# Kernel optimization log

Hardware: AMD Instinct MI355X
Metric: run time of the kernel (lower is better)

The kernel has to match this reference:

```python
import jax, jax.numpy as jnp
import numpy as np

C_IN = 512
OUT_CH = 256  # query/key gate channels
DIM = 64      # squeeze/extraction rank


def setup_inputs() -> dict:
    key = jax.random.key(0)
    ks = jax.random.split(key, 11)
    b, c, h, w = 16, C_IN, 64, 64

    def winit(k, o, i):
        # torch Conv2d default init: U(-s, s), s = 1/sqrt(fan_in)
        s = 1.0 / np.sqrt(i)
        return jax.random.uniform(k, (o, i), jnp.float32, -s, s)

    return {
        "x": jax.random.normal(ks[0], (b, c, h, w), jnp.float32),
        "Wq": winit(ks[1], OUT_CH, C_IN), "bq": winit(ks[2], OUT_CH, C_IN)[:, 0],
        "Wk": winit(ks[3], OUT_CH, C_IN), "bk": winit(ks[4], OUT_CH, C_IN)[:, 0],
        "Wv": winit(ks[5], C_IN, C_IN),   "bv": winit(ks[6], C_IN, C_IN)[:, 0],
        "Ws": winit(ks[7], DIM, C_IN),    "bs": winit(ks[8], DIM, C_IN)[:, 0],
        "We": winit(ks[9], DIM, C_IN),    "be": winit(ks[10], DIM, C_IN)[:, 0],
    }


def reference(x, Wq, bq, Wk, bk, Wv, bv, Ws, bs, We, be):
    b, c, h, w = x.shape
    n = h * w
    xf = x.reshape(b, c, n)  # [b, 512, n] (1x1 conv == matmul over channels)

    Q = jnp.einsum('oc,bcn->bon', Wq, xf) + bq[:, None]   # [b, 256, n]
    K = jnp.einsum('oc,bcn->bon', Wk, xf) + bk[:, None]   # [b, 256, n]
    gate = jax.nn.sigmoid(jnp.mean(Q * K, axis=1, keepdims=True))  # [b, 1, n]

    V = jnp.einsum('oc,bcn->bon', Wv, xf) + bv[:, None]   # [b, 512, n]
    V_dw = V * gate                                        # [b, 512, n]

    Qs = jnp.einsum('oc,bcn->bon', Ws, xf) + bs[:, None]   # [b, 64, n]
    Ke = jnp.einsum('oc,bcn->bon', We, xf) + be[:, None]   # [b, 64, n]

    energy = jnp.einsum('bcn,bdn->bcd', V_dw, Qs)           # [b, 512, 64]
    attention = jax.nn.softmax(energy, axis=-1)
    Vout = jnp.einsum('bcd,bdn->bcn', attention, Ke)        # [b, 512, n]

    return x + Vout.reshape(b, c, h, w)
```

## Files before the change

### kernel.cpp

```cpp
#include <hip/hip_runtime.h>

#define BATCH 16
#define CIN 512
#define NPIX 4096

typedef __attribute__((ext_vector_type(8))) short bf16x8;
typedef __attribute__((ext_vector_type(4))) float f32x4;

#define MFMA(a,b,c) __builtin_amdgcn_mfma_f32_16x16x32_bf16((a),(b),(c),0,0,0)

#define GLOAD(g, l) __builtin_amdgcn_global_load_lds( \
    (const __attribute__((address_space(1))) unsigned int*)(g), \
    (__attribute__((address_space(3))) unsigned int*)(l), 16, 0, 0)

union PK  { short s[8]; bf16x8 v; };
union PK4 { short s[4]; uint2 u; };

__device__ __forceinline__ unsigned short bf16_rne(float f){
  unsigned u = __float_as_uint(f);
  return (unsigned short)((u + 0x7fffu + ((u >> 16) & 1u)) >> 16);
}
__device__ __forceinline__ void f32_split(float f, short &h, short &l){
  unsigned short hu = bf16_rne(f);
  h = (short)hu;
  float fh = __uint_as_float((unsigned)hu << 16);
  l = (short)bf16_rne(f - fh);
}
__device__ __forceinline__ void split8(float4 a, float4 b, bf16x8 &h, bf16x8 &l){
  float vv[8] = {a.x,a.y,a.z,a.w,b.x,b.y,b.z,b.w};
  PK ph, pl;
  #pragma unroll
  for (int z=0;z<8;z++){ short hh,ll; f32_split(vv[z],hh,ll); ph.s[z]=hh; pl.s[z]=ll; }
  h = ph.v; l = pl.v;
}

__device__ __forceinline__ int swz4(int r){ return (r ^ (r >> 2)) & 3; }

__global__ __launch_bounds__(256)
void k_convw(const float* __restrict__ Wq, const float* __restrict__ bq,
             const float* __restrict__ Wk, const float* __restrict__ bk,
             const float* __restrict__ Ws, const float* __restrict__ bs,
             const float* __restrict__ We, const float* __restrict__ be,
             short* __restrict__ WALL2, float* __restrict__ BSE,
             float* __restrict__ VV, float* __restrict__ DD,
             float* __restrict__ QKacc, float* __restrict__ Mb,
             float* __restrict__ Sb){
  int t = blockIdx.x*256 + threadIdx.x;
  if (t < 768*512){
    int r = t >> 9, k = t & 511;
    float v;
    short out;
    if (r < 512){
      v = (r & 1) ? Wk[(r>>1)*512 + k] : Wq[(r>>1)*512 + k];
      out = (short)bf16_rne(v);
    } else if (r < 576){
      short h,l; f32_split(Ws[(r-512)*512 + k], h, l); out = h;
    } else if (r < 640){
      short h,l; f32_split(Ws[(r-576)*512 + k], h, l); out = l;
    } else if (r < 704){
      out = (short)bf16_rne(We[(r-640)*512 + k]);
    } else {
      out = 0;
    }
    int kt = k >> 5, lc = (k >> 3) & 3, e = k & 7;
    int pc = lc ^ swz4(r);
    WALL2[((size_t)kt*768 + r)*32 + pc*8 + e] = out;
  }
  if (t < 128) BSE[t] = (t < 64) ? bs[t] : be[t-64];
  if (t < 512){
    float a = 0.f;
    for (int o=0;o<256;o++) a += bq[o]*Wk[o*512+t] + bk[o]*Wq[o*512+t];
    VV[t] = a;
  }
  if (t == 0){
    float a = 0.f;
    for (int o=0;o<256;o++) a += bq[o]*bk[o];
    DD[0] = a;
  }
  for (int i = t; i < BATCH*NPIX; i += 1536*256) QKacc[i] = 0.f;
  for (int i = t; i < BATCH*512*64; i += 1536*256) Mb[i] = 0.f;
  if (t < BATCH*64) Sb[t] = 0.f;
}

__global__ __launch_bounds__(256)
void k_stage(const float* __restrict__ x, const float* __restrict__ VV,
             short* __restrict__ XT2, float* __restrict__ QKacc){
  __shared__ float XF[64*65];
  int cb = blockIdx.x, nb = blockIdx.y, b = blockIdx.z;
  int tid = threadIdx.x;
  {
    int cc = tid >> 2, ni = (tid & 3) * 16;
    const float* xp = x + ((size_t)(b*CIN + cb*64 + cc))*NPIX + nb*64 + ni;
    #pragma unroll
    for (int u=0;u<16;u+=4){
      float4 v = *(const float4*)(xp + u);
      XF[cc*65 + ni+u+0] = v.x; XF[cc*65 + ni+u+1] = v.y;
      XF[cc*65 + ni+u+2] = v.z; XF[cc*65 + ni+u+3] = v.w;
    }
  }
  __syncthreads();
  {
    int nn = tid >> 2, cs = tid & 3;
    int nl = (nb & 1)*64 + nn, nt = nb >> 1;
    int kt = cb*2 + (cs >> 1);
    float pa = 0.f;
    PK c0, c1;
    #pragma unroll
    for (int i=0;i<8;i++){
      float f = XF[(cs*16 + i)*65 + nn];
      pa += VV[cb*64 + cs*16 + i] * f;
      c0.s[i] = (short)bf16_rne(f);
    }
    #pragma unroll
    for (int i=0;i<8;i++){
      float f = XF[(cs*16 + 8 + i)*65 + nn];
      pa += VV[cb*64 + cs*16 + 8 + i] * f;
      c1.s[i] = (short)bf16_rne(f);
    }
    short* rowb = XT2 + ((((size_t)(b*32 + nt))*16 + kt)*128 + nl)*32;
    int pc0 = ((cs & 1)*2 + 0) ^ swz4(nl);
    int pc1 = ((cs & 1)*2 + 1) ^ swz4(nl);
    *(bf16x8*)&rowb[pc0*8] = c0.v;
    *(bf16x8*)&rowb[pc1*8] = c1.v;
    pa += __shfl_xor(pa, 1);
    pa += __shfl_xor(pa, 2);
    if ((tid & 3) == 0)
      atomicAdd(&QKacc[(size_t)b*NPIX + nb*64 + nn], pa);
  }
}

__global__ __launch_bounds__(256)
void k_gemm12(const short* __restrict__ WALL2, const short* __restrict__ XT2,
              const float* __restrict__ BSE,
              float* __restrict__ QKacc, float* __restrict__ QSR,
              short* __restrict__ KET){
  __shared__ __align__(16) char SMEM[32768];
  short (*As)[128*32] = (short(*)[128*32])SMEM;
  short (*Bs)[128*32] = (short(*)[128*32])(SMEM + 16384);
  __shared__ float QKp[2][2][4][16];
  int nt = blockIdx.x, mt = blockIdx.y, b = blockIdx.z;
  int tid = threadIdx.x, w = tid>>6, lane = tid&63;
  int lr = lane&15, cg = lane>>4;
  int rh = w>>1, nh = w&1;
  const char* Abase = (const char*)WALL2 + (size_t)mt*128*64;
  const char* Bbase = (const char*)XT2 + ((size_t)(b*32 + nt)*16)*8192;
  #pragma unroll
  for (int i=0;i<2;i++){
    GLOAD(Abase + (i*256+tid)*16, ((char*)&As[0][0]) + (i*256+(tid&~63))*16);
    GLOAD(Bbase + (i*256+tid)*16, ((char*)&Bs[0][0]) + (i*256+(tid&~63))*16);
  }
  f32x4 acc[4][4] = {};
  int swz = ((cg ^ swz4(lr)) << 3);
  for (int kt=0; kt<16; kt++){
    int cur = kt & 1;
    __syncthreads();
    if (kt < 15){
      const char* An = Abase + (size_t)(kt+1)*768*64;
      const char* Bn = Bbase + (size_t)(kt+1)*8192;
      #pragma unroll
      for (int i=0;i<2;i++){
        GLOAD(An + (i*256+tid)*16, ((char*)&As[cur^1][0]) + (i*256+(tid&~63))*16);
        GLOAD(Bn + (i*256+tid)*16, ((char*)&Bs[cur^1][0]) + (i*256+(tid&~63))*16);
      }
    }
    bf16x8 a[4], bb[4];
    #pragma unroll
    for (int m=0;m<4;m++) a[m] = *(const bf16x8*)&As[cur][(rh*64 + m*16 + lr)*32 + swz];
    #pragma unroll
    for (int j=0;j<4;j++) bb[j] = *(const bf16x8*)&Bs[cur][(nh*64 + j*16 + lr)*32 + swz];
    #pragma unroll
    for (int m=0;m<4;m++)
      #pragma unroll
      for (int j=0;j<4;j++)
        acc[m][j] = MFMA(a[m], bb[j], acc[m][j]);
  }
  __syncthreads();
  int rq = (lane>>4)<<2;
  if (mt < 4){
    float p[4] = {0.f,0.f,0.f,0.f};
    #pragma unroll
    for (int m=0;m<4;m++)
      #pragma unroll
      for (int j=0;j<4;j++){
        f32x4 a4 = acc[m][j];
        p[j] += a4[0]*a4[1] + a4[2]*a4[3];
      }
    #pragma unroll
    for (int j=0;j<4;j++){ p[j] += __shfl_xor(p[j],16); p[j] += __shfl_xor(p[j],32); }
    if (lane < 16){
      #pragma unroll
      for (int j=0;j<4;j++) QKp[rh][nh][j][lane] = p[j];
    }
    __syncthreads();
    if (rh == 0 && lane < 16){
      #pragma unroll
      for (int j=0;j<4;j++){
        float v = QKp[0][nh][j][lane] + QKp[1][nh][j][lane];
        atomicAdd(&QKacc[(size_t)b*NPIX + nt*128 + nh*64 + j*16 + lane], v);
      }
    }
  } else if (mt == 4){
    float* LO = (float*)SMEM;
    if (rh == 1){
      #pragma unroll
      for (int m=0;m<4;m++)
        #pragma unroll
        for (int j=0;j<4;j++)
          #pragma unroll
          for (int q=0;q<4;q++)
            LO[nh*4096 + (m*16 + rq + q)*64 + j*16 + lr] = acc[m][j][q];
    }
    __syncthreads();
    if (rh == 0){
      #pragma unroll
      for (int m=0;m<4;m++){
        int o0 = m*16 + rq;
        f32x4 bs4 = *(const f32x4*)&BSE[o0];
        #pragma unroll
        for (int j=0;j<4;j++){
          int n = nt*128 + nh*64 + j*16 + lr;
          #pragma unroll
          for (int q=0;q<4;q++)
            QSR[((size_t)(b*64) + o0 + q)*NPIX + n] =
                acc[m][j][q] + LO[nh*4096 + (o0+q)*64 + j*16 + lr] + bs4[q];
        }
      }
    }
  } else {
    if (rh == 0){
      #pragma unroll
      for (int m=0;m<4;m++){
        int d0 = m*16 + rq;
        f32x4 be4 = *(const f32x4*)&BSE[64 + d0];
        #pragma unroll
        for (int j=0;j<4;j++){
          int n = nt*128 + nh*64 + j*16 + lr;
          PK4 pk;
          #pragma unroll
          for (int q=0;q<4;q++) pk.s[q] = (short)bf16_rne(acc[m][j][q] + be4[q]);
          *(uint2*)&KET[((size_t)(b*NPIX) + n)*64 + d0] = pk.u;
        }
      }
    }
  }
}

__global__ __launch_bounds__(256)
void k_gate(const float* __restrict__ QKacc, const float* __restrict__ DD,
            float* __restrict__ GATE){
  int i = blockIdx.x*256 + threadIdx.x;
  GATE[i] = 1.f/(1.f + __expf(-(QKacc[i] + DD[0]) * (1.f/256.f)));
}

__global__ __launch_bounds__(512)
void k_M(const float* __restrict__ x, const float* __restrict__ QSR,
         const float* __restrict__ GATE, float* __restrict__ M,
         float* __restrict__ S){
  int slab = blockIdx.x, b = blockIdx.y;
  int tid = threadIdx.x, w = tid>>6, lane = tid&63;
  int lr = lane&15, lk8 = (lane>>4)<<3;
  f32x4 acc[4][4] = {};
  float srow[4] = {0.f,0.f,0.f,0.f};
  for (int kt=0; kt<8; kt++){
    int noff = slab*256 + kt*32 + lk8;
    const float* gp = GATE + (size_t)b*NPIX + noff;
    float4 g0 = *(const float4*)gp;
    float4 g1 = *(const float4*)(gp + 4);
    bf16x8 bh[4], bl[4];
    #pragma unroll
    for (int j=0;j<4;j++){
      const float* qp = QSR + ((size_t)(b*64) + j*16 + lr)*NPIX + noff;
      float4 q0 = *(const float4*)qp;
      float4 q1 = *(const float4*)(qp+4);
      q0.x *= g0.x; q0.y *= g0.y; q0.z *= g0.z; q0.w *= g0.w;
      q1.x *= g1.x; q1.y *= g1.y; q1.z *= g1.z; q1.w *= g1.w;
      srow[j] += q0.x+q0.y+q0.z+q0.w + q1.x+q1.y+q1.z+q1.w;
      split8(q0, q1, bh[j], bl[j]);
    }
    #pragma unroll
    for (int r=0;r<4;r++){
      const float* xp = x + ((size_t)(b*CIN) + w*64 + r*16 + lr)*NPIX + noff;
      bf16x8 ah, al;
      split8(*(const float4*)xp, *(const float4*)(xp+4), ah, al);
      #pragma unroll
      for (int j=0;j<4;j++){
        acc[r][j] = MFMA(al, bh[j], acc[r][j]);
        acc[r][j] = MFMA(ah, bl[j], acc[r][j]);
        acc[r][j] = MFMA(ah, bh[j], acc[r][j]);
      }
    }
  }
  if (w == 0){
    #pragma unroll
    for (int j=0;j<4;j++){
      float v = srow[j];
      v += __shfl_xor(v, 16);
      v += __shfl_xor(v, 32);
      if (lane < 16) atomicAdd(&S[b*64 + j*16 + lane], v);
    }
  }
  int rq = (lane>>4)<<2;
  #pragma unroll
  for (int r=0;r<4;r++)
    #pragma unroll
    for (int j=0;j<4;j++)
      #pragma unroll
      for (int q=0;q<4;q++)
        atomicAdd(&M[((size_t)(b*CIN) + w*64 + r*16 + rq + q)*64 + j*16 + lr], acc[r][j][q]);
}

__global__ __launch_bounds__(256)
void k_energy(const float* __restrict__ Wv, const float* __restrict__ bv,
              const float* __restrict__ M, const float* __restrict__ S,
              float* __restrict__ EN){
  __shared__ __align__(16) float ML[128*68];
  int cch = blockIdx.x, b = blockIdx.y;
  int tid = threadIdx.x;
  int d4 = tid & 15, ci = tid >> 4;
  f32x4 acc[2] = {};
  for (int kt=0; kt<4; kt++){
    __syncthreads();
    for (int i = tid; i < 2048; i += 256){
      int k = i >> 4, c4 = (i & 15) * 4;
      *(float4*)&ML[k*68 + c4] = *(const float4*)&M[((size_t)(b*CIN) + kt*128 + k)*64 + c4];
    }
    __syncthreads();
    #pragma unroll
    for (int m=0;m<2;m++){
      int c = cch*32 + ci + 16*m;
      const float* wvp = Wv + (size_t)c*512 + kt*128;
      for (int k4=0;k4<32;k4++){
        float4 wv4 = *(const float4*)(wvp + k4*4);
        f32x4 m0 = *(const f32x4*)&ML[(k4*4+0)*68 + d4*4];
        f32x4 m1 = *(const f32x4*)&ML[(k4*4+1)*68 + d4*4];
        f32x4 m2 = *(const f32x4*)&ML[(k4*4+2)*68 + d4*4];
        f32x4 m3 = *(const f32x4*)&ML[(k4*4+3)*68 + d4*4];
        acc[m] += m0*wv4.x + m1*wv4.y + m2*wv4.z + m3*wv4.w;
      }
    }
  }
  f32x4 s4 = *(const f32x4*)&S[b*64 + d4*4];
  #pragma unroll
  for (int m=0;m<2;m++){
    int c = cch*32 + ci + 16*m;
    f32x4 r = acc[m] + s4*bv[c];
    *(f32x4*)&EN[((size_t)(b*CIN) + c)*64 + d4*4] = r;
  }
}

__global__ __launch_bounds__(256)
void k_softmax(const float* __restrict__ EN, short* __restrict__ ATT){
  int row = blockIdx.x*4 + (threadIdx.x>>6);
  int lane = threadIdx.x & 63;
  float v = EN[(size_t)row*64 + lane];
  float m = v;
  #pragma unroll
  for (int s=1;s<64;s<<=1) m = fmaxf(m, __shfl_xor(m, s));
  float e = __expf(v - m);
  float sum = e;
  #pragma unroll
  for (int s=1;s<64;s<<=1) sum += __shfl_xor(sum, s);
  ATT[(size_t)row*64 + lane] = (short)bf16_rne(e / sum);
}

__global__ __launch_bounds__(512)
void k_out(const float* __restrict__ x, const short* __restrict__ ATT,
           const short* __restrict__ KET, float* __restrict__ out){
  __shared__ __align__(16) float CT[256*66];
  int nt = blockIdx.x, b = blockIdx.y;
  int n0 = nt*64;
  int tid = threadIdx.x, w = tid>>6, lane = tid&63;
  int lr = lane&15, lk = (lane>>4)<<3;
  f32x4 acc[4][4] = {};
  #pragma unroll
  for (int kt=0; kt<2; kt++){
    bf16x8 bb[4];
    #pragma unroll
    for (int j=0;j<4;j++)
      bb[j] = *(const bf16x8*)&KET[((size_t)(b*NPIX) + n0 + j*16 + lr)*64 + kt*32 + lk];
    #pragma unroll
    for (int r=0;r<4;r++){
      bf16x8 a = *(const bf16x8*)&ATT[((size_t)(b*CIN) + w*64 + r*16 + lr)*64 + kt*32 + lk];
      #pragma unroll
      for (int j=0;j<4;j++)
        acc[r][j] = MFMA(a, bb[j], acc[r][j]);
    }
  }
  int rq = (lane>>4)<<2;
  #pragma unroll
  for (int pass=0; pass<2; pass++){
    __syncthreads();
    if ((w>>2) == pass){
      int wl = w & 3;
      #pragma unroll
      for (int r=0;r<4;r++)
        #pragma unroll
        for (int j=0;j<4;j++)
          #pragma unroll
          for (int q=0;q<4;q++)
            CT[(wl*64 + r*16 + rq + q)*66 + j*16 + lr] = acc[r][j][q];
    }
    __syncthreads();
    #pragma unroll
    for (int i0=0; i0<2; i0++){
      int i = i0*512 + tid;
      int row = i >> 2, seg = (i & 3)*16;
      size_t gidx = ((size_t)(b*CIN) + pass*256 + row)*NPIX + n0 + seg;
      const float* cp = &CT[row*66 + seg];
      const float* xp = &x[gidx];
      float* op = &out[gidx];
      #pragma unroll
      for (int u=0;u<4;u++){
        f32x4 c4 = *(const f32x4*)(cp + u*4);
        f32x4 x4 = *(const f32x4*)(xp + u*4);
        *(f32x4*)(op + u*4) = c4 + x4;
      }
    }
  }
}

extern "C" void kernel_launch(void* const* d_in, const int* in_sizes, int n_in,
                              void* d_out, int out_size, void* d_ws, size_t ws_size,
                              hipStream_t stream){
  const float* x   = (const float*)d_in[0];
  const float* Wq  = (const float*)d_in[1];
  const float* bq  = (const float*)d_in[2];
  const float* Wk  = (const float*)d_in[3];
  const float* bk  = (const float*)d_in[4];
  const float* Wv  = (const float*)d_in[5];
  const float* bv  = (const float*)d_in[6];
  const float* Wsq = (const float*)d_in[7];
  const float* bsq = (const float*)d_in[8];
  const float* We  = (const float*)d_in[9];
  const float* be  = (const float*)d_in[10];
  float* out = (float*)d_out;

  char* wsb = (char*)d_ws;
  size_t off = 0;
  auto alloc = [&](size_t bytes)->void*{
    void* p = wsb + off; off += (bytes + 255) & ~(size_t)255; return p;
  };
  short* WALL2= (short*)alloc((size_t)768*512*2);
  float* BSE  = (float*)alloc(128*4);
  float* VV   = (float*)alloc(512*4);
  float* DD   = (float*)alloc(256);
  short* XT2  = (short*)alloc((size_t)BATCH*NPIX*512*2);
  float* QKacc= (float*)alloc((size_t)BATCH*NPIX*4);
  float* GATE = (float*)alloc((size_t)BATCH*NPIX*4);
  float* QSR  = (float*)alloc((size_t)BATCH*64*NPIX*4);
  short* KET  = (short*)alloc((size_t)BATCH*NPIX*64*2);
  float* Mb   = (float*)alloc((size_t)BATCH*512*64*4);
  float* Sb   = (float*)alloc((size_t)BATCH*64*4);
  float* EN   = (float*)alloc((size_t)BATCH*512*64*4);
  short* ATT  = (short*)alloc((size_t)BATCH*512*64*2);

  k_convw  <<<1536, 256, 0, stream>>>(Wq,bq,Wk,bk,Wsq,bsq,We,be, WALL2,BSE,VV,DD,
                                      QKacc, Mb, Sb);
  k_stage  <<<dim3(8,64,16), 256, 0, stream>>>(x, VV, XT2, QKacc);
  k_gemm12 <<<dim3(32,6,16), 256, 0, stream>>>(WALL2, XT2, BSE, QKacc, QSR, KET);
  k_gate   <<<256, 256, 0, stream>>>(QKacc, DD, GATE);
  k_M      <<<dim3(16,16), 512, 0, stream>>>(x, QSR, GATE, Mb, Sb);
  k_energy <<<dim3(16,16), 256, 0, stream>>>(Wv, bv, Mb, Sb, EN);
  k_softmax<<<2048, 256, 0, stream>>>(EN, ATT);
  k_out    <<<dim3(64,16), 512, 0, stream>>>(x, ATT, KET, out);
}
```

Baseline: 279.1 us.

## Fuse gate sigmoid into k_M and softmax into k_out; unroll VV reduction

Removes the separate gate and softmax kernels. The sigmoid gate is now computed inline in k_M from QKacc, and each k_out block recomputes the softmax of its batch's 512x64 energy rows into swizzled LDS before its MFMA. The VV bias reduction in k_convw gets four accumulators and unrolling. This saves two launches and the GATE/ATT round trips, but k_out now redoes the full per-batch softmax in each of its 64 blocks per batch, 64 serial rows per wave.

```diff
diff --git a/kernel.cpp b/kernel.cpp
--- a/kernel.cpp
+++ b/kernel.cpp
@@ -35,6 +35,11 @@
 }
 
 __device__ __forceinline__ int swz4(int r){ return (r ^ (r >> 2)) & 3; }
+__device__ __forceinline__ int off128(int row, int k){
+  int s = k >> 3;
+  s = (s & ~7) | ((s ^ row) & 7);
+  return row*64 + s*8 + (k & 7);
+}
 
 __global__ __launch_bounds__(256)
 void k_convw(const float* __restrict__ Wq, const float* __restrict__ bq,
@@ -68,9 +73,15 @@
   }
   if (t < 128) BSE[t] = (t < 64) ? bs[t] : be[t-64];
   if (t < 512){
-    float a = 0.f;
-    for (int o=0;o<256;o++) a += bq[o]*Wk[o*512+t] + bk[o]*Wq[o*512+t];
-    VV[t] = a;
+    float a0=0.f, a1=0.f, a2=0.f, a3=0.f;
+    #pragma unroll 8
+    for (int o=0;o<256;o+=4){
+      a0 += bq[o+0]*Wk[(o+0)*512+t] + bk[o+0]*Wq[(o+0)*512+t];
+      a1 += bq[o+1]*Wk[(o+1)*512+t] + bk[o+1]*Wq[(o+1)*512+t];
+      a2 += bq[o+2]*Wk[(o+2)*512+t] + bk[o+2]*Wq[(o+2)*512+t];
+      a3 += bq[o+3]*Wk[(o+3)*512+t] + bk[o+3]*Wq[(o+3)*512+t];
+    }
+    VV[t] = (a0+a1)+(a2+a3);
   }
   if (t == 0){
     float a = 0.f;
@@ -245,27 +256,30 @@
   }
 }
 
-__global__ __launch_bounds__(256)
-void k_gate(const float* __restrict__ QKacc, const float* __restrict__ DD,
-            float* __restrict__ GATE){
-  int i = blockIdx.x*256 + threadIdx.x;
-  GATE[i] = 1.f/(1.f + __expf(-(QKacc[i] + DD[0]) * (1.f/256.f)));
-}
-
 __global__ __launch_bounds__(512)
 void k_M(const float* __restrict__ x, const float* __restrict__ QSR,
-         const float* __restrict__ GATE, float* __restrict__ M,
-         float* __restrict__ S){
+         const float* __restrict__ QKacc, const float* __restrict__ DD,
+         float* __restrict__ M, float* __restrict__ S){
   int slab = blockIdx.x, b = blockIdx.y;
   int tid = threadIdx.x, w = tid>>6, lane = tid&63;
   int lr = lane&15, lk8 = (lane>>4)<<3;
+  float dd = DD[0];
   f32x4 acc[4][4] = {};
   float srow[4] = {0.f,0.f,0.f,0.f};
   for (int kt=0; kt<8; kt++){
     int noff = slab*256 + kt*32 + lk8;
-    const float* gp = GATE + (size_t)b*NPIX + noff;
-    float4 g0 = *(const float4*)gp;
-    float4 g1 = *(const float4*)(gp + 4);
+    const float* qkp = QKacc + (size_t)b*NPIX + noff;
+    float4 k0 = *(const float4*)qkp;
+    float4 k1 = *(const float4*)(qkp + 4);
+    float4 g0, g1;
+    g0.x = 1.f/(1.f + __expf(-(k0.x+dd)*(1.f/256.f)));
+    g0.y = 1.f/(1.f + __expf(-(k0.y+dd)*(1.f/256.f)));
+    g0.z = 1.f/(1.f + __expf(-(k0.z+dd)*(1.f/256.f)));
+    g0.w = 1.f/(1.f + __expf(-(k0.w+dd)*(1.f/256.f)));
+    g1.x = 1.f/(1.f + __expf(-(k1.x+dd)*(1.f/256.f)));
+    g1.y = 1.f/(1.f + __expf(-(k1.y+dd)*(1.f/256.f)));
+    g1.z = 1.f/(1.f + __expf(-(k1.z+dd)*(1.f/256.f)));
+    g1.w = 1.f/(1.f + __expf(-(k1.w+dd)*(1.f/256.f)));
     bf16x8 bh[4], bl[4];
     #pragma unroll
     for (int j=0;j<4;j++){
@@ -348,29 +362,29 @@
   }
 }
 
-__global__ __launch_bounds__(256)
-void k_softmax(const float* __restrict__ EN, short* __restrict__ ATT){
-  int row = blockIdx.x*4 + (threadIdx.x>>6);
-  int lane = threadIdx.x & 63;
-  float v = EN[(size_t)row*64 + lane];
-  float m = v;
-  #pragma unroll
-  for (int s=1;s<64;s<<=1) m = fmaxf(m, __shfl_xor(m, s));
-  float e = __expf(v - m);
-  float sum = e;
-  #pragma unroll
-  for (int s=1;s<64;s<<=1) sum += __shfl_xor(sum, s);
-  ATT[(size_t)row*64 + lane] = (short)bf16_rne(e / sum);
-}
-
 __global__ __launch_bounds__(512)
-void k_out(const float* __restrict__ x, const short* __restrict__ ATT,
+void k_out(const float* __restrict__ x, const float* __restrict__ EN,
            const short* __restrict__ KET, float* __restrict__ out){
-  __shared__ __align__(16) float CT[256*66];
+  __shared__ __align__(16) char SM[67584];
+  short* AT = (short*)SM;
+  float* CT = (float*)SM;
   int nt = blockIdx.x, b = blockIdx.y;
   int n0 = nt*64;
   int tid = threadIdx.x, w = tid>>6, lane = tid&63;
   int lr = lane&15, lk = (lane>>4)<<3;
+  for (int i=0;i<64;i++){
+    int row = w*64 + i;
+    float v = EN[((size_t)(b*CIN) + row)*64 + lane];
+    float m = v;
+    #pragma unroll
+    for (int s=1;s<64;s<<=1) m = fmaxf(m, __shfl_xor(m, s));
+    float e = __expf(v - m);
+    float sum = e;
+    #pragma unroll
+    for (int s=1;s<64;s<<=1) sum += __shfl_xor(sum, s);
+    AT[off128(row, lane)] = (short)bf16_rne(e / sum);
+  }
+  __syncthreads();
   f32x4 acc[4][4] = {};
   #pragma unroll
   for (int kt=0; kt<2; kt++){
@@ -380,7 +394,7 @@
       bb[j] = *(const bf16x8*)&KET[((size_t)(b*NPIX) + n0 + j*16 + lr)*64 + kt*32 + lk];
     #pragma unroll
     for (int r=0;r<4;r++){
-      bf16x8 a = *(const bf16x8*)&ATT[((size_t)(b*CIN) + w*64 + r*16 + lr)*64 + kt*32 + lk];
+      bf16x8 a = *(const bf16x8*)&AT[off128(w*64 + r*16 + lr, kt*32 + lk)];
       #pragma unroll
       for (int j=0;j<4;j++)
         acc[r][j] = MFMA(a, bb[j], acc[r][j]);
@@ -446,21 +460,17 @@
   float* DD   = (float*)alloc(256);
   short* XT2  = (short*)alloc((size_t)BATCH*NPIX*512*2);
   float* QKacc= (float*)alloc((size_t)BATCH*NPIX*4);
-  float* GATE = (float*)alloc((size_t)BATCH*NPIX*4);
   float* QSR  = (float*)alloc((size_t)BATCH*64*NPIX*4);
   short* KET  = (short*)alloc((size_t)BATCH*NPIX*64*2);
   float* Mb   = (float*)alloc((size_t)BATCH*512*64*4);
   float* Sb   = (float*)alloc((size_t)BATCH*64*4);
   float* EN   = (float*)alloc((size_t)BATCH*512*64*4);
-  short* ATT  = (short*)alloc((size_t)BATCH*512*64*2);
 
   k_convw  <<<1536, 256, 0, stream>>>(Wq,bq,Wk,bk,Wsq,bsq,We,be, WALL2,BSE,VV,DD,
                                       QKacc, Mb, Sb);
   k_stage  <<<dim3(8,64,16), 256, 0, stream>>>(x, VV, XT2, QKacc);
   k_gemm12 <<<dim3(32,6,16), 256, 0, stream>>>(WALL2, XT2, BSE, QKacc, QSR, KET);
-  k_gate   <<<256, 256, 0, stream>>>(QKacc, DD, GATE);
-  k_M      <<<dim3(16,16), 512, 0, stream>>>(x, QSR, GATE, Mb, Sb);
+  k_M      <<<dim3(16,16), 512, 0, stream>>>(x, QSR, QKacc, DD, Mb, Sb);
   k_energy <<<dim3(16,16), 256, 0, stream>>>(Wv, bv, Mb, Sb, EN);
-  k_softmax<<<2048, 256, 0, stream>>>(EN, ATT);
-  k_out    <<<dim3(64,16), 512, 0, stream>>>(x, ATT, KET, out);
-}
+  k_out    <<<dim3(64,16), 512, 0, stream>>>(x, EN, KET, out);
+}
```

Result: slower. 364.1 us (+30.5%).
